# Performance work log

Hardware: AMD Instinct MI355X
Metric: run time of the kernel (lower is better)

Reference implementation:

```python
import jax, jax.numpy as jnp
import numpy as np
from jax import lax

EPS = 1e-5
DN = ('NCHW', 'OIHW', 'NCHW')


def binarize(x):
    # sign(x) with 0 -> +1, matching _STESign.forward
    return jnp.where(x >= 0, jnp.ones_like(x), -jnp.ones_like(x))


def batchnorm(x, g, b, m, v):
    # inference BatchNorm2d with running stats
    scale = (g / jnp.sqrt(v + EPS))[None, :, None, None]
    shift = (b - m * g / jnp.sqrt(v + EPS))[None, :, None, None]
    return x * scale + shift


def conv(x, w, stride):
    return lax.conv_general_dilated(x, w, (stride, stride), [(1, 1), (1, 1)],
                                    dimension_numbers=DN)


def setup_inputs() -> dict:
    key = jax.random.key(0)
    ks = jax.random.split(key, 24)
    d = {}
    d['x'] = jax.random.normal(ks[0], (32, 3, 224, 224), dtype=jnp.float32)
    d['conv1_w'] = jax.random.normal(ks[1], (32, 3, 3, 3), dtype=jnp.float32) * 0.1
    d['conv2_w'] = jax.random.normal(ks[2], (64, 32, 3, 3), dtype=jnp.float32) * 0.1
    d['conv3_w'] = jax.random.normal(ks[3], (128, 64, 3, 3), dtype=jnp.float32) * 0.1
    d['conv4_w'] = jax.random.normal(ks[4], (256, 128, 3, 3), dtype=jnp.float32) * 0.1
    for i, c in zip(range(1, 5), (32, 64, 128, 256)):
        base = 4 + (i - 1) * 4
        d[f'bn{i}_g'] = jax.random.uniform(ks[base + 1], (c,), dtype=jnp.float32) + 0.5
        d[f'bn{i}_b'] = jax.random.normal(ks[base + 2], (c,), dtype=jnp.float32) * 0.1
        d[f'bn{i}_m'] = jax.random.normal(ks[base + 3], (c,), dtype=jnp.float32) * 0.1
        d[f'bn{i}_v'] = jax.random.uniform(ks[base + 4], (c,), dtype=jnp.float32) + 0.5
    d['fc_w'] = jax.random.normal(ks[21], (2, 256), dtype=jnp.float32) * 0.05
    d['fc_b'] = jnp.zeros((2,), dtype=jnp.float32)
    return d


def reference(x, conv1_w, conv2_w, conv3_w, conv4_w,
              bn1_g, bn1_b, bn1_m, bn1_v,
              bn2_g, bn2_b, bn2_m, bn2_v,
              bn3_g, bn3_b, bn3_m, bn3_v,
              bn4_g, bn4_b, bn4_m, bn4_v,
              fc_w, fc_b):
    # conv1 (real) + bn1
    h = batchnorm(conv(x, conv1_w, 1), bn1_g, bn1_b, bn1_m, bn1_v)
    # BinarizeConv2d: binarize input and weight, then real conv
    h = binarize(batchnorm(conv(binarize(h), binarize(conv2_w), 2), bn2_g, bn2_b, bn2_m, bn2_v))
    h = binarize(batchnorm(conv(binarize(h), binarize(conv3_w), 2), bn3_g, bn3_b, bn3_m, bn3_v))
    h = binarize(batchnorm(conv(binarize(h), binarize(conv4_w), 2), bn4_g, bn4_b, bn4_m, bn4_v))
    # adaptive avg pool to 1x1 -> mean over H,W
    h = jnp.mean(h, axis=(2, 3))  # [B, 256]
    return h @ fc_w.T + fc_b
```

## Files before the change

kernel.cpp:

```cpp
#include <hip/hip_runtime.h>
#include <stdint.h>
#include <math.h>

#define OFF_S1     0
#define OFF_W1T    256
#define OFF_T2     3712
#define OFF_P2     3968
#define OFF_T3     4224
#define OFF_P3     4736
#define OFF_T4     5248
#define OFF_P4     6272
#define OFF_W2     7296
#define OFF_W3     9600
#define OFF_W4     18816
#define OFF_A1     55680
#define OFF_A2     6478208
#define OFF_A3     9689472
#define OFF_A4     11295104

static __device__ __forceinline__ float2 bnf(float g, float b, float m, float v) {
    float sc = __fdiv_rn(g, __fsqrt_rn(__fadd_rn(v, 1e-5f)));
    float sh = __fsub_rn(b, __fmul_rn(m, sc));
    return make_float2(sc, sh);
}
static __device__ __forceinline__ bool bnpos(float s, float2 p) {
    return __fadd_rn(__fmul_rn(s, p.x), p.y) >= 0.0f;
}
static __device__ __forceinline__ int find_T(int K, float2 p) {
    int lo = -K - 2, hi = K + 2;
    while (lo + 2 < hi) {
        int mid = ((lo + hi) >> 1) & ~1;
        if (bnpos((float)mid, p)) hi = mid; else lo = mid;
    }
    return hi;
}

__global__ __launch_bounds__(256) void k_prep(
    const float* __restrict__ w1, const float* __restrict__ w2,
    const float* __restrict__ w3, const float* __restrict__ w4,
    const float* g1, const float* b1, const float* m1, const float* v1,
    const float* g2, const float* b2, const float* m2, const float* v2,
    const float* g3, const float* b3, const float* m3, const float* v3,
    const float* g4, const float* b4, const float* m4, const float* v4,
    float2* __restrict__ S1, float* __restrict__ W1T,
    int* __restrict__ T2, int* __restrict__ P2,
    int* __restrict__ T3, int* __restrict__ P3,
    int* __restrict__ T4, int* __restrict__ P4,
    uint32_t* __restrict__ W2, uint64_t* __restrict__ W3, uint64_t* __restrict__ W4)
{
    int gtid = blockIdx.x * 256 + threadIdx.x;
    int wid  = gtid >> 6;
    int lane = gtid & 63;

    if (wid < 576) {
        int oc = wid / 9, t = wid - oc * 9;
        float v = (lane < 32) ? w2[oc * 288 + lane * 9 + t] : -1.0f;
        uint64_t m = __ballot(v >= 0.0f);
        if (lane == 0) W2[wid] = (uint32_t)m;
    } else if (wid < 1728) {
        int i = wid - 576;
        int oc = i / 9, t = i - oc * 9;
        float v = w3[oc * 576 + lane * 9 + t];
        uint64_t m = __ballot(v >= 0.0f);
        if (lane == 0) W3[i] = m;
    } else if (wid < 6336) {
        int i = wid - 1728;
        int oc = i / 18, rem = i - oc * 18;
        int t = rem >> 1, h = rem & 1;
        float v = w4[oc * 1152 + (h * 64 + lane) * 9 + t];
        uint64_t m = __ballot(v >= 0.0f);
        if (lane == 0) W4[i] = m;
    } else {
        int t = gtid - 405504;
        if (t < 864) {
            int k = t >> 5, oc = t & 31;
            W1T[t] = w1[oc * 27 + k];
        } else if (t < 896) {
            int c = t - 864;
            S1[c] = bnf(g1[c], b1[c], m1[c], v1[c]);
        } else if (t < 960) {
            int c = t - 896;
            int T = find_T(288, bnf(g2[c], b2[c], m2[c], v2[c]));
            T2[c] = T; P2[c] = (288 - T) >> 1;
        } else if (t < 1088) {
            int c = t - 960;
            int T = find_T(576, bnf(g3[c], b3[c], m3[c], v3[c]));
            T3[c] = T; P3[c] = (576 - T) >> 1;
        } else if (t < 1344) {
            int c = t - 1088;
            int T = find_T(1152, bnf(g4[c], b4[c], m4[c], v4[c]));
            T4[c] = T; P4[c] = (1152 - T) >> 1;
        }
    }
}

__global__ __launch_bounds__(256) void k_conv1(
    const float* __restrict__ x, const float* __restrict__ w1,
    const float2* __restrict__ S1g, uint32_t* __restrict__ A1)
{
    __shared__ float  wl[27 * 32];
    __shared__ float2 s1[32];
    int tid = threadIdx.x;
    for (int i = tid; i < 864; i += 256) {
        int k = i >> 5, oc = i & 31;
        wl[i] = w1[oc * 27 + k];
    }
    if (tid < 32) s1[tid] = S1g[tid];
    __syncthreads();

    int idx = blockIdx.x * 256 + tid;
    int xp = idx % 112;
    int t  = idx / 112;
    int y  = t % 224;
    int b  = t / 224;
    int xc = xp * 2;

    const float* xb = x + (size_t)b * 3 * 50176;
    float xin[3][3][4];
    #pragma unroll
    for (int ic = 0; ic < 3; ic++)
        #pragma unroll
        for (int ky = 0; ky < 3; ky++)
            #pragma unroll
            for (int cx = 0; cx < 4; cx++) {
                int iy = y - 1 + ky, ix = xc - 1 + cx;
                float v = 0.0f;
                if ((unsigned)iy < 224u && (unsigned)ix < 224u)
                    v = xb[ic * 50176 + iy * 224 + ix];
                xin[ic][ky][cx] = v;
            }

    float acc0[32], acc1[32];
    #pragma unroll
    for (int oc = 0; oc < 32; oc++) { acc0[oc] = 0.0f; acc1[oc] = 0.0f; }

    const float4* wl4 = (const float4*)wl;
    #pragma unroll
    for (int k = 0; k < 27; k++) {
        int ic = k / 9, r = (k % 9) / 3, c = k % 3;
        float a0 = xin[ic][r][c];
        float a1 = xin[ic][r][c + 1];
        #pragma unroll
        for (int g8 = 0; g8 < 8; g8++) {
            float4 w = wl4[k * 8 + g8];
            acc0[g8 * 4 + 0] = fmaf(a0, w.x, acc0[g8 * 4 + 0]);
            acc0[g8 * 4 + 1] = fmaf(a0, w.y, acc0[g8 * 4 + 1]);
            acc0[g8 * 4 + 2] = fmaf(a0, w.z, acc0[g8 * 4 + 2]);
            acc0[g8 * 4 + 3] = fmaf(a0, w.w, acc0[g8 * 4 + 3]);
            acc1[g8 * 4 + 0] = fmaf(a1, w.x, acc1[g8 * 4 + 0]);
            acc1[g8 * 4 + 1] = fmaf(a1, w.y, acc1[g8 * 4 + 1]);
            acc1[g8 * 4 + 2] = fmaf(a1, w.z, acc1[g8 * 4 + 2]);
            acc1[g8 * 4 + 3] = fmaf(a1, w.w, acc1[g8 * 4 + 3]);
        }
    }

    uint32_t bits0 = 0, bits1 = 0;
    #pragma unroll
    for (int oc = 0; oc < 32; oc++) {
        bits0 |= (uint32_t)bnpos(acc0[oc], s1[oc]) << oc;
        bits1 |= (uint32_t)bnpos(acc1[oc], s1[oc]) << oc;
    }
    uint2* dst = (uint2*)(A1 + (size_t)b * 50176 + y * 224 + xc);
    *dst = make_uint2(bits0, bits1);
}

#define C2_LW 114
#define C3_LW 57
#define C4_LW 29

template<unsigned VM>
static __device__ __forceinline__ bool px2(const uint32_t* row, int c0,
                                           const uint32_t* wreg, int T) {
    int pc = 0;
    #pragma unroll
    for (int ky = 0; ky < 3; ky++)
        #pragma unroll
        for (int kx = 0; kx < 3; kx++) {
            int ti = ky * 3 + kx;
            if (VM & (1u << ti))
                pc += __popc(row[ky * C2_LW + c0 + kx] ^ wreg[ti]);
        }
    const int nv = ((VM>>0)&1)+((VM>>1)&1)+((VM>>2)&1)+((VM>>3)&1)+((VM>>4)&1)
                 + ((VM>>5)&1)+((VM>>6)&1)+((VM>>7)&1)+((VM>>8)&1);
    return pc <= ((32 * nv - T) >> 1);
}

template<unsigned VM>
static __device__ __forceinline__ bool px3(const uint64_t* row, int c0,
                                           const uint64_t* wreg, int T) {
    int pc = 0;
    #pragma unroll
    for (int ky = 0; ky < 3; ky++)
        #pragma unroll
        for (int kx = 0; kx < 3; kx++) {
            int ti = ky * 3 + kx;
            if (VM & (1u << ti))
                pc += __popcll(row[ky * C3_LW + c0 + kx] ^ wreg[ti]);
        }
    const int nv = ((VM>>0)&1)+((VM>>1)&1)+((VM>>2)&1)+((VM>>3)&1)+((VM>>4)&1)
                 + ((VM>>5)&1)+((VM>>6)&1)+((VM>>7)&1)+((VM>>8)&1);
    return pc <= ((64 * nv - T) >> 1);
}

template<unsigned VM>
static __device__ __forceinline__ bool px4(const uint64_t* base, int c0,
                                           const ulonglong2* wreg, int T) {
    int pc = 0;
    #pragma unroll
    for (int ky = 0; ky < 3; ky++)
        #pragma unroll
        for (int kx = 0; kx < 3; kx++) {
            int ti = ky * 3 + kx;
            if (VM & (1u << ti)) {
                int a = (ky * C4_LW + c0 + kx) * 2;
                pc += __popcll(base[a] ^ wreg[ti].x);
                pc += __popcll(base[a + 1] ^ wreg[ti].y);
            }
        }
    const int nv = ((VM>>0)&1)+((VM>>1)&1)+((VM>>2)&1)+((VM>>3)&1)+((VM>>4)&1)
                 + ((VM>>5)&1)+((VM>>6)&1)+((VM>>7)&1)+((VM>>8)&1);
    return pc <= ((128 * nv - T) >> 1);
}

__global__ __launch_bounds__(256) void k_conv2(
    const uint32_t* __restrict__ A1, const uint32_t* __restrict__ W2g,
    const int* __restrict__ T2, uint64_t* __restrict__ A2)
{
    __shared__ uint32_t lds[9 * C2_LW];
    int bi = blockIdx.x;
    int b = bi / 56, rem = bi % 56;
    int oyq = rem >> 1, h = rem & 1;
    int xs = h * 56;
    int tid = threadIdx.x;
    const uint32_t* ap = A1 + (size_t)b * 50176;
    for (int i = tid; i < 9 * C2_LW; i += 256) {
        int r = i / C2_LW, c = i - r * C2_LW;
        int iy = oyq * 8 - 1 + r, ix = 2 * xs - 1 + c;
        uint32_t v = 0;
        if ((unsigned)iy < 224u && (unsigned)ix < 224u) v = ap[iy * 224 + ix];
        lds[i] = v;
    }
    __syncthreads();

    int w = tid >> 6, lane = tid & 63;
    int oy = oyq * 4 + w;
    uint32_t wreg[9];
    #pragma unroll
    for (int ti = 0; ti < 9; ti++) wreg[ti] = W2g[lane * 9 + ti];
    int T = T2[lane];
    const uint32_t* lrow = lds + 2 * w * C2_LW;
    uint64_t* dst = A2 + (size_t)b * 12544 + oy * 112 + xs;
    bool left = (xs == 0);

    if (oy == 0) {
        int lx0 = 0;
        if (left) {
            uint64_t wd = __ballot(px2<0x1B0>(lrow, 0, wreg, T));
            if (lane == 0) dst[0] = wd;
            lx0 = 1;
        }
        for (int lx = lx0; lx < 56; lx++) {
            uint64_t wd = __ballot(px2<0x1F8>(lrow, 2 * lx, wreg, T));
            if (lane == 0) dst[lx] = wd;
        }
    } else {
        int lx0 = 0;
        if (left) {
            uint64_t wd = __ballot(px2<0x1B6>(lrow, 0, wreg, T));
            if (lane == 0) dst[0] = wd;
            lx0 = 1;
        }
        for (int lx = lx0; lx < 56; lx++) {
            uint64_t wd = __ballot(px2<0x1FF>(lrow, 2 * lx, wreg, T));
            if (lane == 0) dst[lx] = wd;
        }
    }
}

__global__ __launch_bounds__(256) void k_conv3(
    const uint64_t* __restrict__ A2, const uint64_t* __restrict__ W3g,
    const int* __restrict__ T3, uint64_t* __restrict__ A3)
{
    __shared__ uint64_t lds[5 * C3_LW];
    int bi = blockIdx.x;
    int b = bi / 56, rem = bi % 56;
    int oyp = rem >> 1, h = rem & 1;
    int xs = h * 28;
    int tid = threadIdx.x;
    const uint64_t* ap = A2 + (size_t)b * 12544;
    for (int i = tid; i < 5 * C3_LW; i += 256) {
        int r = i / C3_LW, c = i - r * C3_LW;
        int iy = oyp * 4 - 1 + r, ix = 2 * xs - 1 + c;
        uint64_t v = 0;
        if ((unsigned)iy < 112u && (unsigned)ix < 112u) v = ap[iy * 112 + ix];
        lds[i] = v;
    }
    __syncthreads();

    int w = tid >> 6, lane = tid & 63;
    int oy = oyp * 2 + (w >> 1);
    int g  = w & 1;
    int oc = g * 64 + lane;
    uint64_t wreg[9];
    #pragma unroll
    for (int ti = 0; ti < 9; ti++) wreg[ti] = W3g[oc * 9 + ti];
    int T = T3[oc];
    const uint64_t* lrow = lds + 2 * (w >> 1) * C3_LW;
    uint64_t* dst = A3 + (size_t)g * 100352 + (size_t)b * 3136 + oy * 56 + xs;
    bool left = (xs == 0);

    if (oy == 0) {
        int lx0 = 0;
        if (left) {
            uint64_t wd = __ballot(px3<0x1B0>(lrow, 0, wreg, T));
            if (lane == 0) dst[0] = wd;
            lx0 = 1;
        }
        for (int lx = lx0; lx < 28; lx++) {
            uint64_t wd = __ballot(px3<0x1F8>(lrow, 2 * lx, wreg, T));
            if (lane == 0) dst[lx] = wd;
        }
    } else {
        int lx0 = 0;
        if (left) {
            uint64_t wd = __ballot(px3<0x1B6>(lrow, 0, wreg, T));
            if (lane == 0) dst[0] = wd;
            lx0 = 1;
        }
        for (int lx = lx0; lx < 28; lx++) {
            uint64_t wd = __ballot(px3<0x1FF>(lrow, 2 * lx, wreg, T));
            if (lane == 0) dst[lx] = wd;
        }
    }
}

__global__ __launch_bounds__(256) void k_conv4(
    const uint64_t* __restrict__ A3, const uint64_t* __restrict__ W4g,
    const int* __restrict__ T4, uint64_t* __restrict__ A4)
{
    __shared__ uint64_t lds[3 * C4_LW * 2];
    int bi = blockIdx.x;
    int b = bi / 56, rem = bi % 56;
    int oy = rem >> 1, h = rem & 1;
    int xs = h * 14;
    int tid = threadIdx.x;
    const uint64_t* ap = A3 + (size_t)b * 3136;
    for (int i = tid; i < 3 * C4_LW * 2; i += 256) {
        int pl = i & 1, j = i >> 1;
        int r = j / C4_LW, c = j - r * C4_LW;
        int iy = 2 * oy - 1 + r, ix = 2 * xs - 1 + c;
        uint64_t v = 0;
        if ((unsigned)iy < 56u && (unsigned)ix < 56u)
            v = ap[(size_t)pl * 100352 + iy * 56 + ix];
        lds[(r * C4_LW + c) * 2 + pl] = v;
    }
    __syncthreads();

    int w = tid >> 6, lane = tid & 63;
    int oc = w * 64 + lane;
    ulonglong2 wreg[9];
    const ulonglong2* wp = (const ulonglong2*)(W4g + oc * 18);
    #pragma unroll
    for (int ti = 0; ti < 9; ti++) wreg[ti] = wp[ti];
    int T = T4[oc];
    uint64_t* dst = A4 + (size_t)w * 25088 + (size_t)b * 784 + oy * 28 + xs;
    bool left = (xs == 0);

    if (oy == 0) {
        int lx0 = 0;
        if (left) {
            uint64_t wd = __ballot(px4<0x1B0>(lds, 0, wreg, T));
            if (lane == 0) dst[0] = wd;
            lx0 = 1;
        }
        for (int lx = lx0; lx < 14; lx++) {
            uint64_t wd = __ballot(px4<0x1F8>(lds, 2 * lx, wreg, T));
            if (lane == 0) dst[lx] = wd;
        }
    } else {
        int lx0 = 0;
        if (left) {
            uint64_t wd = __ballot(px4<0x1B6>(lds, 0, wreg, T));
            if (lane == 0) dst[0] = wd;
            lx0 = 1;
        }
        for (int lx = lx0; lx < 14; lx++) {
            uint64_t wd = __ballot(px4<0x1FF>(lds, 2 * lx, wreg, T));
            if (lane == 0) dst[lx] = wd;
        }
    }
}

__global__ __launch_bounds__(1024) void k_tail(
    const uint64_t* __restrict__ A4, const float* __restrict__ fcw,
    const float* __restrict__ fcb, float* __restrict__ out)
{
    int b = blockIdx.x;
    int tid = threadIdx.x;
    int c = tid & 255, chunk = tid >> 8;
    int g = c >> 6, bit = c & 63;
    const uint64_t* base = A4 + (size_t)g * 25088 + (size_t)b * 784;
    int cnt = 0;
    for (int p = chunk * 196; p < (chunk + 1) * 196; p++)
        cnt += (int)((base[p] >> bit) & 1ull);

    __shared__ int cnts[4][256];
    __shared__ double r0[256], r1[256];
    cnts[chunk][c] = cnt;
    __syncthreads();
    if (tid < 256) {
        int tot = cnts[0][c] + cnts[1][c] + cnts[2][c] + cnts[3][c];
        double mean = (2.0 * (double)tot - 784.0) * (1.0 / 784.0);
        r0[c] = (double)fcw[c]       * mean;
        r1[c] = (double)fcw[256 + c] * mean;
    }
    __syncthreads();
    for (int s = 128; s > 0; s >>= 1) {
        if (tid < s) { r0[tid] += r0[tid + s]; r1[tid] += r1[tid + s]; }
        __syncthreads();
    }
    if (tid == 0) {
        out[b * 2 + 0] = (float)(r0[0] + (double)fcb[0]);
        out[b * 2 + 1] = (float)(r1[0] + (double)fcb[1]);
    }
}

extern "C" void kernel_launch(void* const* d_in, const int* in_sizes, int n_in,
                              void* d_out, int out_size, void* d_ws, size_t ws_size,
                              hipStream_t stream) {
    const float* x   = (const float*)d_in[0];
    const float* w1  = (const float*)d_in[1];
    const float* w2  = (const float*)d_in[2];
    const float* w3  = (const float*)d_in[3];
    const float* w4  = (const float*)d_in[4];
    const float* g1 = (const float*)d_in[5],  *b1 = (const float*)d_in[6],
               * m1 = (const float*)d_in[7],  *v1 = (const float*)d_in[8];
    const float* g2 = (const float*)d_in[9],  *b2 = (const float*)d_in[10],
               * m2 = (const float*)d_in[11], *v2 = (const float*)d_in[12];
    const float* g3 = (const float*)d_in[13], *b3 = (const float*)d_in[14],
               * m3 = (const float*)d_in[15], *v3 = (const float*)d_in[16];
    const float* g4 = (const float*)d_in[17], *b4 = (const float*)d_in[18],
               * m4 = (const float*)d_in[19], *v4 = (const float*)d_in[20];
    const float* fcw = (const float*)d_in[21];
    const float* fcb = (const float*)d_in[22];
    float* out = (float*)d_out;

    char* ws = (char*)d_ws;
    float2*   S1  = (float2*)(ws + OFF_S1);
    float*    W1T = (float*)(ws + OFF_W1T);
    int*      T2  = (int*)(ws + OFF_T2);
    int*      P2  = (int*)(ws + OFF_P2);
    int*      T3  = (int*)(ws + OFF_T3);
    int*      P3  = (int*)(ws + OFF_P3);
    int*      T4  = (int*)(ws + OFF_T4);
    int*      P4  = (int*)(ws + OFF_P4);
    uint32_t* W2  = (uint32_t*)(ws + OFF_W2);
    uint64_t* W3  = (uint64_t*)(ws + OFF_W3);
    uint64_t* W4  = (uint64_t*)(ws + OFF_W4);
    uint32_t* A1  = (uint32_t*)(ws + OFF_A1);
    uint64_t* A2  = (uint64_t*)(ws + OFF_A2);
    uint64_t* A3  = (uint64_t*)(ws + OFF_A3);
    uint64_t* A4  = (uint64_t*)(ws + OFF_A4);

    hipLaunchKernelGGL(k_prep, dim3(1590), dim3(256), 0, stream,
                       w1, w2, w3, w4,
                       g1, b1, m1, v1, g2, b2, m2, v2,
                       g3, b3, m3, v3, g4, b4, m4, v4,
                       S1, W1T, T2, P2, T3, P3, T4, P4, W2, W3, W4);
    hipLaunchKernelGGL(k_conv1, dim3(3136), dim3(256), 0, stream, x, w1, S1, A1);
    hipLaunchKernelGGL(k_conv2, dim3(1792), dim3(256), 0, stream, A1, W2, T2, A2);
    hipLaunchKernelGGL(k_conv3, dim3(1792), dim3(256), 0, stream, A2, W3, T3, A3);
    hipLaunchKernelGGL(k_conv4, dim3(1792), dim3(256), 0, stream, A3, W4, T4, A4);
    hipLaunchKernelGGL(k_tail,  dim3(32),   dim3(1024), 0, stream, A4, fcw, fcb, out);
}
```

Before: 239.2 us.

## Register-tile binary conv windows, vectorize LDS reads and output stores

The binary conv kernels now load a sliding window of LDS words into registers once per group of output pixels, using vector loads, and reuse it across 4 (conv2/conv3) or 2 (conv4) stride-2 outputs. Ballot results are written as 128-bit stores. conv4's LDS layout changes from interleaved planes to separate planes. conv1 gets a fast interior path that skips per-element bounds checks, and the tail kernel reads A4 with 128-bit loads. The goal is fewer redundant LDS reads and narrow stores, at the cost of more register pressure.

```diff
diff --git a/kernel.cpp b/kernel.cpp
--- a/kernel.cpp
+++ b/kernel.cpp
@@ -117,18 +117,29 @@
 
     const float* xb = x + (size_t)b * 3 * 50176;
     float xin[3][3][4];
-    #pragma unroll
-    for (int ic = 0; ic < 3; ic++)
+    if ((unsigned)(y - 1) < 222u && (unsigned)(xp - 1) < 110u) {
         #pragma unroll
-        for (int ky = 0; ky < 3; ky++)
+        for (int ic = 0; ic < 3; ic++)
             #pragma unroll
-            for (int cx = 0; cx < 4; cx++) {
-                int iy = y - 1 + ky, ix = xc - 1 + cx;
-                float v = 0.0f;
-                if ((unsigned)iy < 224u && (unsigned)ix < 224u)
-                    v = xb[ic * 50176 + iy * 224 + ix];
-                xin[ic][ky][cx] = v;
+            for (int ky = 0; ky < 3; ky++) {
+                const float* rp = xb + ic * 50176 + (y - 1 + ky) * 224 + (xc - 1);
+                #pragma unroll
+                for (int cx = 0; cx < 4; cx++) xin[ic][ky][cx] = rp[cx];
             }
+    } else {
+        #pragma unroll
+        for (int ic = 0; ic < 3; ic++)
+            #pragma unroll
+            for (int ky = 0; ky < 3; ky++)
+                #pragma unroll
+                for (int cx = 0; cx < 4; cx++) {
+                    int iy = y - 1 + ky, ix = xc - 1 + cx;
+                    float v = 0.0f;
+                    if ((unsigned)iy < 224u && (unsigned)ix < 224u)
+                        v = xb[ic * 50176 + iy * 224 + ix];
+                    xin[ic][ky][cx] = v;
+                }
+    }
 
     float acc0[32], acc1[32];
     #pragma unroll
@@ -166,60 +177,47 @@
 
 #define C2_LW 114
 #define C3_LW 57
-#define C4_LW 29
 
 template<unsigned VM>
-static __device__ __forceinline__ bool px2(const uint32_t* row, int c0,
-                                           const uint32_t* wreg, int T) {
+static __device__ __forceinline__ bool pred2(const uint32_t (&w)[3][9], int j,
+                                             const uint32_t (&wr)[9], int T) {
     int pc = 0;
     #pragma unroll
     for (int ky = 0; ky < 3; ky++)
         #pragma unroll
         for (int kx = 0; kx < 3; kx++) {
             int ti = ky * 3 + kx;
-            if (VM & (1u << ti))
-                pc += __popc(row[ky * C2_LW + c0 + kx] ^ wreg[ti]);
+            if (VM & (1u << ti)) pc += __popc(w[ky][2 * j + kx] ^ wr[ti]);
         }
-    const int nv = ((VM>>0)&1)+((VM>>1)&1)+((VM>>2)&1)+((VM>>3)&1)+((VM>>4)&1)
-                 + ((VM>>5)&1)+((VM>>6)&1)+((VM>>7)&1)+((VM>>8)&1);
+    constexpr int nv = __builtin_popcount(VM);
     return pc <= ((32 * nv - T) >> 1);
 }
 
-template<unsigned VM>
-static __device__ __forceinline__ bool px3(const uint64_t* row, int c0,
-                                           const uint64_t* wreg, int T) {
-    int pc = 0;
-    #pragma unroll
-    for (int ky = 0; ky < 3; ky++)
-        #pragma unroll
-        for (int kx = 0; kx < 3; kx++) {
-            int ti = ky * 3 + kx;
-            if (VM & (1u << ti))
-                pc += __popcll(row[ky * C3_LW + c0 + kx] ^ wreg[ti]);
-        }
-    const int nv = ((VM>>0)&1)+((VM>>1)&1)+((VM>>2)&1)+((VM>>3)&1)+((VM>>4)&1)
-                 + ((VM>>5)&1)+((VM>>6)&1)+((VM>>7)&1)+((VM>>8)&1);
-    return pc <= ((64 * nv - T) >> 1);
-}
-
-template<unsigned VM>
-static __device__ __forceinline__ bool px4(const uint64_t* base, int c0,
-                                           const ulonglong2* wreg, int T) {
-    int pc = 0;
-    #pragma unroll
-    for (int ky = 0; ky < 3; ky++)
-        #pragma unroll
-        for (int kx = 0; kx < 3; kx++) {
-            int ti = ky * 3 + kx;
-            if (VM & (1u << ti)) {
-                int a = (ky * C4_LW + c0 + kx) * 2;
-                pc += __popcll(base[a] ^ wreg[ti].x);
-                pc += __popcll(base[a + 1] ^ wreg[ti].y);
-            }
-        }
-    const int nv = ((VM>>0)&1)+((VM>>1)&1)+((VM>>2)&1)+((VM>>3)&1)+((VM>>4)&1)
-                 + ((VM>>5)&1)+((VM>>6)&1)+((VM>>7)&1)+((VM>>8)&1);
-    return pc <= ((128 * nv - T) >> 1);
+template<unsigned VM0, unsigned VM>
+static __device__ __forceinline__ void group2(const uint32_t* lrow, int g,
+        const uint32_t (&wr)[9], int T, uint64_t* dst, int lane) {
+    uint32_t win[3][9];
+    int c0 = 8 * g;
+    #pragma unroll
+    for (int r = 0; r < 3; r++) {
+        const uint32_t* rp = lrow + r * C2_LW + c0;
+        uint2 a0 = *(const uint2*)(rp);
+        uint2 a1 = *(const uint2*)(rp + 2);
+        uint2 a2 = *(const uint2*)(rp + 4);
+        uint2 a3 = *(const uint2*)(rp + 6);
+        win[r][0] = a0.x; win[r][1] = a0.y; win[r][2] = a1.x; win[r][3] = a1.y;
+        win[r][4] = a2.x; win[r][5] = a2.y; win[r][6] = a3.x; win[r][7] = a3.y;
+        win[r][8] = rp[8];
+    }
+    uint64_t b0 = __ballot(pred2<VM0>(win, 0, wr, T));
+    uint64_t b1 = __ballot(pred2<VM >(win, 1, wr, T));
+    uint64_t b2 = __ballot(pred2<VM >(win, 2, wr, T));
+    uint64_t b3 = __ballot(pred2<VM >(win, 3, wr, T));
+    if (lane == 0) {
+        ulonglong2* d = (ulonglong2*)(dst + 4 * g);
+        d[0] = make_ulonglong2(b0, b1);
+        d[1] = make_ulonglong2(b2, b3);
+    }
 }
 
 __global__ __launch_bounds__(256) void k_conv2(
@@ -244,36 +242,64 @@
 
     int w = tid >> 6, lane = tid & 63;
     int oy = oyq * 4 + w;
-    uint32_t wreg[9];
-    #pragma unroll
-    for (int ti = 0; ti < 9; ti++) wreg[ti] = W2g[lane * 9 + ti];
+    uint32_t wr[9];
+    #pragma unroll
+    for (int ti = 0; ti < 9; ti++) wr[ti] = W2g[lane * 9 + ti];
     int T = T2[lane];
     const uint32_t* lrow = lds + 2 * w * C2_LW;
     uint64_t* dst = A2 + (size_t)b * 12544 + oy * 112 + xs;
     bool left = (xs == 0);
 
     if (oy == 0) {
-        int lx0 = 0;
-        if (left) {
-            uint64_t wd = __ballot(px2<0x1B0>(lrow, 0, wreg, T));
-            if (lane == 0) dst[0] = wd;
-            lx0 = 1;
+        if (left) group2<0x1B0, 0x1F8>(lrow, 0, wr, T, dst, lane);
+        else      group2<0x1F8, 0x1F8>(lrow, 0, wr, T, dst, lane);
+        for (int g = 1; g < 14; g++) group2<0x1F8, 0x1F8>(lrow, g, wr, T, dst, lane);
+    } else {
+        if (left) group2<0x1B6, 0x1FF>(lrow, 0, wr, T, dst, lane);
+        else      group2<0x1FF, 0x1FF>(lrow, 0, wr, T, dst, lane);
+        for (int g = 1; g < 14; g++) group2<0x1FF, 0x1FF>(lrow, g, wr, T, dst, lane);
+    }
+}
+
+template<unsigned VM>
+static __device__ __forceinline__ bool pred3(const uint64_t (&w)[3][9], int j,
+                                             const uint64_t (&wr)[9], int T) {
+    int pc = 0;
+    #pragma unroll
+    for (int ky = 0; ky < 3; ky++)
+        #pragma unroll
+        for (int kx = 0; kx < 3; kx++) {
+            int ti = ky * 3 + kx;
+            if (VM & (1u << ti)) pc += __popcll(w[ky][2 * j + kx] ^ wr[ti]);
         }
-        for (int lx = lx0; lx < 56; lx++) {
-            uint64_t wd = __ballot(px2<0x1F8>(lrow, 2 * lx, wreg, T));
-            if (lane == 0) dst[lx] = wd;
-        }
-    } else {
-        int lx0 = 0;
-        if (left) {
-            uint64_t wd = __ballot(px2<0x1B6>(lrow, 0, wreg, T));
-            if (lane == 0) dst[0] = wd;
-            lx0 = 1;
-        }
-        for (int lx = lx0; lx < 56; lx++) {
-            uint64_t wd = __ballot(px2<0x1FF>(lrow, 2 * lx, wreg, T));
-            if (lane == 0) dst[lx] = wd;
-        }
+    constexpr int nv = __builtin_popcount(VM);
+    return pc <= ((64 * nv - T) >> 1);
+}
+
+template<unsigned VM0, unsigned VM>
+static __device__ __forceinline__ void group3(const uint64_t* lrow, int g,
+        const uint64_t (&wr)[9], int T, uint64_t* dst, int lane) {
+    uint64_t win[3][9];
+    int c0 = 8 * g;
+    #pragma unroll
+    for (int r = 0; r < 3; r++) {
+        const uint64_t* rp = lrow + r * C3_LW + c0;
+        ulonglong2 a0 = *(const ulonglong2*)(rp);
+        ulonglong2 a1 = *(const ulonglong2*)(rp + 2);
+        ulonglong2 a2 = *(const ulonglong2*)(rp + 4);
+        ulonglong2 a3 = *(const ulonglong2*)(rp + 6);
+        win[r][0] = a0.x; win[r][1] = a0.y; win[r][2] = a1.x; win[r][3] = a1.y;
+        win[r][4] = a2.x; win[r][5] = a2.y; win[r][6] = a3.x; win[r][7] = a3.y;
+        win[r][8] = rp[8];
+    }
+    uint64_t b0 = __ballot(pred3<VM0>(win, 0, wr, T));
+    uint64_t b1 = __ballot(pred3<VM >(win, 1, wr, T));
+    uint64_t b2 = __ballot(pred3<VM >(win, 2, wr, T));
+    uint64_t b3 = __ballot(pred3<VM >(win, 3, wr, T));
+    if (lane == 0) {
+        ulonglong2* d = (ulonglong2*)(dst + 4 * g);
+        d[0] = make_ulonglong2(b0, b1);
+        d[1] = make_ulonglong2(b2, b3);
     }
 }
 
@@ -301,93 +327,108 @@
     int oy = oyp * 2 + (w >> 1);
     int g  = w & 1;
     int oc = g * 64 + lane;
-    uint64_t wreg[9];
-    #pragma unroll
-    for (int ti = 0; ti < 9; ti++) wreg[ti] = W3g[oc * 9 + ti];
+    uint64_t wr[9];
+    #pragma unroll
+    for (int ti = 0; ti < 9; ti++) wr[ti] = W3g[oc * 9 + ti];
     int T = T3[oc];
     const uint64_t* lrow = lds + 2 * (w >> 1) * C3_LW;
     uint64_t* dst = A3 + (size_t)g * 100352 + (size_t)b * 3136 + oy * 56 + xs;
     bool left = (xs == 0);
 
     if (oy == 0) {
-        int lx0 = 0;
-        if (left) {
-            uint64_t wd = __ballot(px3<0x1B0>(lrow, 0, wreg, T));
-            if (lane == 0) dst[0] = wd;
-            lx0 = 1;
+        if (left) group3<0x1B0, 0x1F8>(lrow, 0, wr, T, dst, lane);
+        else      group3<0x1F8, 0x1F8>(lrow, 0, wr, T, dst, lane);
+        for (int gg = 1; gg < 7; gg++) group3<0x1F8, 0x1F8>(lrow, gg, wr, T, dst, lane);
+    } else {
+        if (left) group3<0x1B6, 0x1FF>(lrow, 0, wr, T, dst, lane);
+        else      group3<0x1FF, 0x1FF>(lrow, 0, wr, T, dst, lane);
+        for (int gg = 1; gg < 7; gg++) group3<0x1FF, 0x1FF>(lrow, gg, wr, T, dst, lane);
+    }
+}
+
+template<unsigned VM>
+static __device__ __forceinline__ bool pred4(const uint64_t (&w0)[3][5],
+                                             const uint64_t (&w1)[3][5], int j,
+                                             const ulonglong2 (&wr)[9], int T) {
+    int pc = 0;
+    #pragma unroll
+    for (int ky = 0; ky < 3; ky++)
+        #pragma unroll
+        for (int kx = 0; kx < 3; kx++) {
+            int ti = ky * 3 + kx;
+            if (VM & (1u << ti)) {
+                pc += __popcll(w0[ky][2 * j + kx] ^ wr[ti].x);
+                pc += __popcll(w1[ky][2 * j + kx] ^ wr[ti].y);
+            }
         }
-        for (int lx = lx0; lx < 28; lx++) {
-            uint64_t wd = __ballot(px3<0x1F8>(lrow, 2 * lx, wreg, T));
-            if (lane == 0) dst[lx] = wd;
-        }
-    } else {
-        int lx0 = 0;
-        if (left) {
-            uint64_t wd = __ballot(px3<0x1B6>(lrow, 0, wreg, T));
-            if (lane == 0) dst[0] = wd;
-            lx0 = 1;
-        }
-        for (int lx = lx0; lx < 28; lx++) {
-            uint64_t wd = __ballot(px3<0x1FF>(lrow, 2 * lx, wreg, T));
-            if (lane == 0) dst[lx] = wd;
-        }
-    }
+    constexpr int nv = __builtin_popcount(VM);
+    return pc <= ((128 * nv - T) >> 1);
+}
+
+template<unsigned VM0, unsigned VM>
+static __device__ __forceinline__ void group4(const uint64_t* ldsb, int g,
+        const ulonglong2 (&wr)[9], int T, uint64_t* dst, int lane) {
+    uint64_t w0[3][5], w1[3][5];
+    int c0 = 4 * g;
+    #pragma unroll
+    for (int r = 0; r < 3; r++) {
+        const uint64_t* rp0 = ldsb + r * 30 + c0;
+        const uint64_t* rp1 = ldsb + (3 + r) * 30 + c0;
+        ulonglong2 a0 = *(const ulonglong2*)(rp0);
+        ulonglong2 a1 = *(const ulonglong2*)(rp0 + 2);
+        w0[r][0] = a0.x; w0[r][1] = a0.y; w0[r][2] = a1.x; w0[r][3] = a1.y;
+        w0[r][4] = rp0[4];
+        ulonglong2 b0 = *(const ulonglong2*)(rp1);
+        ulonglong2 b1 = *(const ulonglong2*)(rp1 + 2);
+        w1[r][0] = b0.x; w1[r][1] = b0.y; w1[r][2] = b1.x; w1[r][3] = b1.y;
+        w1[r][4] = rp1[4];
+    }
+    uint64_t r0 = __ballot(pred4<VM0>(w0, w1, 0, wr, T));
+    uint64_t r1 = __ballot(pred4<VM >(w0, w1, 1, wr, T));
+    if (lane == 0)
+        *(ulonglong2*)(dst + 2 * g) = make_ulonglong2(r0, r1);
 }
 
 __global__ __launch_bounds__(256) void k_conv4(
     const uint64_t* __restrict__ A3, const uint64_t* __restrict__ W4g,
     const int* __restrict__ T4, uint64_t* __restrict__ A4)
 {
-    __shared__ uint64_t lds[3 * C4_LW * 2];
+    __shared__ uint64_t lds[2 * 3 * 30];
     int bi = blockIdx.x;
     int b = bi / 56, rem = bi % 56;
     int oy = rem >> 1, h = rem & 1;
     int xs = h * 14;
     int tid = threadIdx.x;
     const uint64_t* ap = A3 + (size_t)b * 3136;
-    for (int i = tid; i < 3 * C4_LW * 2; i += 256) {
-        int pl = i & 1, j = i >> 1;
-        int r = j / C4_LW, c = j - r * C4_LW;
+    for (int i = tid; i < 174; i += 256) {
+        int p = i / 87, j = i - p * 87;
+        int r = j / 29, c = j - r * 29;
         int iy = 2 * oy - 1 + r, ix = 2 * xs - 1 + c;
         uint64_t v = 0;
         if ((unsigned)iy < 56u && (unsigned)ix < 56u)
-            v = ap[(size_t)pl * 100352 + iy * 56 + ix];
-        lds[(r * C4_LW + c) * 2 + pl] = v;
+            v = ap[(size_t)p * 100352 + iy * 56 + ix];
+        lds[(p * 3 + r) * 30 + c] = v;
     }
     __syncthreads();
 
     int w = tid >> 6, lane = tid & 63;
     int oc = w * 64 + lane;
-    ulonglong2 wreg[9];
+    ulonglong2 wr[9];
     const ulonglong2* wp = (const ulonglong2*)(W4g + oc * 18);
     #pragma unroll
-    for (int ti = 0; ti < 9; ti++) wreg[ti] = wp[ti];
+    for (int ti = 0; ti < 9; ti++) wr[ti] = wp[ti];
     int T = T4[oc];
     uint64_t* dst = A4 + (size_t)w * 25088 + (size_t)b * 784 + oy * 28 + xs;
     bool left = (xs == 0);
 
     if (oy == 0) {
-        int lx0 = 0;
-        if (left) {
-            uint64_t wd = __ballot(px4<0x1B0>(lds, 0, wreg, T));
-            if (lane == 0) dst[0] = wd;
-            lx0 = 1;
-        }
-        for (int lx = lx0; lx < 14; lx++) {
-            uint64_t wd = __ballot(px4<0x1F8>(lds, 2 * lx, wreg, T));
-            if (lane == 0) dst[lx] = wd;
-        }
+        if (left) group4<0x1B0, 0x1F8>(lds, 0, wr, T, dst, lane);
+        else      group4<0x1F8, 0x1F8>(lds, 0, wr, T, dst, lane);
+        for (int g = 1; g < 7; g++) group4<0x1F8, 0x1F8>(lds, g, wr, T, dst, lane);
     } else {
-        int lx0 = 0;
-        if (left) {
-            uint64_t wd = __ballot(px4<0x1B6>(lds, 0, wreg, T));
-            if (lane == 0) dst[0] = wd;
-            lx0 = 1;
-        }
-        for (int lx = lx0; lx < 14; lx++) {
-            uint64_t wd = __ballot(px4<0x1FF>(lds, 2 * lx, wreg, T));
-            if (lane == 0) dst[lx] = wd;
-        }
+        if (left) group4<0x1B6, 0x1FF>(lds, 0, wr, T, dst, lane);
+        else      group4<0x1FF, 0x1FF>(lds, 0, wr, T, dst, lane);
+        for (int g = 1; g < 7; g++) group4<0x1FF, 0x1FF>(lds, g, wr, T, dst, lane);
     }
 }
 
@@ -399,10 +440,13 @@
     int tid = threadIdx.x;
     int c = tid & 255, chunk = tid >> 8;
     int g = c >> 6, bit = c & 63;
-    const uint64_t* base = A4 + (size_t)g * 25088 + (size_t)b * 784;
+    const uint64_t* base = A4 + (size_t)g * 25088 + (size_t)b * 784 + chunk * 196;
+    const ulonglong2* bp = (const ulonglong2*)base;
     int cnt = 0;
-    for (int p = chunk * 196; p < (chunk + 1) * 196; p++)
-        cnt += (int)((base[p] >> bit) & 1ull);
+    for (int i = 0; i < 98; i++) {
+        ulonglong2 v = bp[i];
+        cnt += (int)((v.x >> bit) & 1ull) + (int)((v.y >> bit) & 1ull);
+    }
 
     __shared__ int cnts[4][256];
     __shared__ double r0[256], r1[256];
```

New measurement: 244.7 us. +2.3%, slower.
